# Kernel tuning notes

Hardware: AMD Instinct MI355X
Metric: run time of the kernel (lower is better)

The kernel has to match this reference:

```python
import jax, jax.numpy as jnp
import numpy as np

B, N, D = 8, 4096, 256
T = 768          # text_dim
E = 4            # num_experts
K = 2            # top_k
GS = 64          # grid_size = img_size // patch_size
WS = 8           # swin window size
NH = 4           # swin heads
MODES = 16       # fno modes
HID = 4 * D      # mlp hidden


def setup_inputs() -> dict:
    key = jax.random.key(0)
    ks = jax.random.split(key, 40)
    rn = lambda k, s, sc=0.02: jax.random.normal(k, s, jnp.float32) * sc
    return {
        "x": jax.random.normal(ks[0], (B, N, D), jnp.float32),
        "text_embedding": jax.random.normal(ks[1], (B, T), jnp.float32),
        # TopKGating: Linear(D+T->D), ReLU, Linear(D->E)
        "g1_w": rn(ks[2], (D, D + T)), "g1_b": jnp.zeros((D,), jnp.float32),
        "g2_w": rn(ks[3], (E, D)), "g2_b": jnp.zeros((E,), jnp.float32),
        # FNOExpert: SpectralConv2d complex weights (real/imag) + 1x1 conv
        "fno_w1r": rn(ks[4], (D, D, MODES, MODES), 1.0 / D), "fno_w1i": rn(ks[5], (D, D, MODES, MODES), 1.0 / D),
        "fno_w2r": rn(ks[6], (D, D, MODES, MODES), 1.0 / D), "fno_w2i": rn(ks[7], (D, D, MODES, MODES), 1.0 / D),
        "fno_cw": rn(ks[8], (D, D)), "fno_cb": jnp.zeros((D,), jnp.float32),
        # MLPExpert #1
        "m1_w1": rn(ks[9], (HID, D)), "m1_b1": jnp.zeros((HID,), jnp.float32),
        "m1_w2": rn(ks[10], (D, HID)), "m1_b2": jnp.zeros((D,), jnp.float32),
        # WindowAttentionExpert
        "a_ln1w": jnp.ones((D,), jnp.float32), "a_ln1b": jnp.zeros((D,), jnp.float32),
        "a_qkvw": rn(ks[11], (3 * D, D)), "a_qkvb": jnp.zeros((3 * D,), jnp.float32),
        "a_ow": rn(ks[12], (D, D)), "a_ob": jnp.zeros((D,), jnp.float32),
        "a_ln2w": jnp.ones((D,), jnp.float32), "a_ln2b": jnp.zeros((D,), jnp.float32),
        "a_mw1": rn(ks[13], (HID, D)), "a_mb1": jnp.zeros((HID,), jnp.float32),
        "a_mw2": rn(ks[14], (D, HID)), "a_mb2": jnp.zeros((D,), jnp.float32),
        # MLPExpert #2 (extra expert to reach num_experts=4)
        "m2_w1": rn(ks[15], (HID, D)), "m2_b1": jnp.zeros((HID,), jnp.float32),
        "m2_w2": rn(ks[16], (D, HID)), "m2_b2": jnp.zeros((D,), jnp.float32),
    }


def _gelu(v):
    return jax.nn.gelu(v, approximate=False)


def _ln(v, g, b, eps=1e-5):
    m = v.mean(-1, keepdims=True)
    var = ((v - m) ** 2).mean(-1, keepdims=True)
    return (v - m) * jax.lax.rsqrt(var + eps) * g + b


def reference(x, text_embedding, g1_w, g1_b, g2_w, g2_b,
              fno_w1r, fno_w1i, fno_w2r, fno_w2i, fno_cw, fno_cb,
              m1_w1, m1_b1, m1_w2, m1_b2,
              a_ln1w, a_ln1b, a_qkvw, a_qkvb, a_ow, a_ob,
              a_ln2w, a_ln2b, a_mw1, a_mb1, a_mw2, a_mb2,
              m2_w1, m2_b1, m2_w2, m2_b2):
    Bb, Nn, Dd = x.shape

    # ---- TopKGating ----
    feat = jnp.concatenate([x.mean(axis=1), text_embedding], axis=1)   # [B, D+T]
    h = jax.nn.relu(feat @ g1_w.T + g1_b)
    logits = h @ g2_w.T + g2_b                                         # [B, E]
    vals, idx = jax.lax.top_k(logits, K)
    w = jax.nn.softmax(vals, axis=1)                                   # [B, K]
    # per-(sample, expert) combine weight; indices are constants
    combine = (w[..., None] * jax.nn.one_hot(idx, E, dtype=x.dtype)).sum(axis=1)  # [B, E]

    # ---- Expert 0: FNO ----
    def fno(v):
        xg = v.transpose(0, 2, 1).reshape(Bb, Dd, GS, GS)              # [B, D, H, W]
        xft = jnp.fft.rfft2(xg)                                        # [B, D, H, W//2+1]
        w1 = fno_w1r + 1j * fno_w1i
        w2 = fno_w2r + 1j * fno_w2i
        lo = jnp.einsum('bixy,ioxy->boxy', xft[:, :, :MODES, :MODES], w1)
        hi = jnp.einsum('bixy,ioxy->boxy', xft[:, :, -MODES:, :MODES], w2)
        out_ft = jnp.zeros_like(xft)
        out_ft = out_ft.at[:, :, :MODES, :MODES].set(lo)
        out_ft = out_ft.at[:, :, -MODES:, :MODES].set(hi)
        x1 = jnp.fft.irfft2(out_ft, s=(GS, GS))
        x2 = jnp.einsum('bihw,oi->bohw', xg, fno_cw) + fno_cb[None, :, None, None]
        out = _gelu(x1 + x2)
        return out.reshape(Bb, Dd, Nn).transpose(0, 2, 1) + v

    # ---- MLP experts ----
    def mlp(v, w1, b1, w2, b2):
        return _gelu(v @ w1.T + b1) @ w2.T + b2 + v

    # ---- Expert 2: window attention ----
    def win_attn(v):
        xs = _ln(v, a_ln1w, a_ln1b).reshape(Bb, GS, GS, Dd)
        nw = GS // WS
        xw = xs.reshape(Bb, nw, WS, nw, WS, Dd).transpose(0, 1, 3, 2, 4, 5)
        xw = xw.reshape(-1, WS * WS, Dd)                               # [B*nw*nw, L, D]
        qkv = xw @ a_qkvw.T + a_qkvb
        q, k, vv = jnp.split(qkv, 3, axis=-1)
        dh = Dd // NH
        heads = lambda t: t.reshape(-1, WS * WS, NH, dh).transpose(0, 2, 1, 3)
        q, k, vv = heads(q), heads(k), heads(vv)
        attn = jax.nn.softmax(q @ k.transpose(0, 1, 3, 2) / jnp.sqrt(jnp.float32(dh)), axis=-1)
        o = (attn @ vv).transpose(0, 2, 1, 3).reshape(-1, WS * WS, Dd) @ a_ow.T + a_ob
        o = o.reshape(Bb, nw, nw, WS, WS, Dd).transpose(0, 1, 3, 2, 4, 5).reshape(Bb, Nn, Dd)
        v2 = v + o
        return v2 + (_gelu(_ln(v2, a_ln2w, a_ln2b) @ a_mw1.T + a_mb1) @ a_mw2.T + a_mb2)

    outs = [fno(x),
            mlp(x, m1_w1, m1_b1, m1_w2, m1_b2),
            win_attn(x),
            mlp(x, m2_w1, m2_b1, m2_w2, m2_b2)]
    final = sum(combine[:, e, None, None] * outs[e] for e in range(E))
    return final, w
```

## Files before the change

### kernel.cpp

```cpp
#include <hip/hip_runtime.h>
#include <math.h>

#define BB 8
#define NN 4096
#define DDIM 256
#define TT 768
#define BND (BB*NN*DDIM)

typedef unsigned short ushort_t;
typedef short bf16x8 __attribute__((ext_vector_type(8)));
typedef float f32x4 __attribute__((ext_vector_type(4)));

__device__ __forceinline__ float gelu_f(float v){
    return 0.5f * v * (1.0f + erff(v * 0.70710678118654752f));
}
__device__ __forceinline__ ushort_t f2bf(float f){
    union { float f; unsigned int u; } v; v.f = f;
    unsigned int u = v.u;
    u += 0x7FFFu + ((u >> 16) & 1u);
    return (ushort_t)(u >> 16);
}
__device__ __forceinline__ float bf2f(ushort_t h){
    union { unsigned int u; float f; } v; v.u = ((unsigned int)h) << 16;
    return v.f;
}
__device__ __forceinline__ float pk_re(unsigned int p){
    union { unsigned int u; float f; } v; v.u = p << 16; return v.f;
}
__device__ __forceinline__ float pk_im(unsigned int p){
    union { unsigned int u; float f; } v; v.u = p & 0xffff0000u; return v.f;
}
#define GLOAD16(gp, lp) __builtin_amdgcn_global_load_lds( \
    (__attribute__((address_space(1))) const void*)(gp),  \
    (__attribute__((address_space(3))) void*)(lp), 16, 0, 0)

__global__ __launch_bounds__(256) void k_xcvt2(const float4* __restrict__ x,
    const float* __restrict__ lng, const float* __restrict__ lnb,
    ushort_t* __restrict__ xbf, ushort_t* __restrict__ xlnbf, float4* __restrict__ outp,
    float* __restrict__ partialA){
    int w = threadIdx.x >> 6, lane = threadIdx.x & 63;
    int row = blockIdx.x*4 + w;
    size_t i4 = (size_t)row*64 + lane;
    float4 v = x[i4];
    outp[i4] = v;
    float vv[4] = {v.x, v.y, v.z, v.w};
    __shared__ float sda[4][256];
    *(float4*)&sda[w][lane*4] = v;
    float s = (vv[0]+vv[1])+(vv[2]+vv[3]);
    float s2 = (vv[0]*vv[0]+vv[1]*vv[1])+(vv[2]*vv[2]+vv[3]*vv[3]);
    for (int off=32; off; off>>=1){ s += __shfl_down(s, off); s2 += __shfl_down(s2, off); }
    float m = __shfl(s, 0) * (1.0f/DDIM);
    float var = __shfl(s2, 0) * (1.0f/DDIM) - m*m;
    float r = rsqrtf(var + 1e-5f);
    int c0 = lane*4;
    #pragma unroll
    for (int u=0;u<4;++u){
        size_t i = i4*4 + u;
        xbf[i] = f2bf(vv[u]);
        xlnbf[i] = f2bf((vv[u]-m)*r*lng[c0+u] + lnb[c0+u]);
    }
    __syncthreads();
    if (w==0){
        float4 a = *(const float4*)&sda[0][lane*4];
        float4 b4 = *(const float4*)&sda[1][lane*4];
        float4 c4 = *(const float4*)&sda[2][lane*4];
        float4 d4 = *(const float4*)&sda[3][lane*4];
        float4 sum = make_float4(a.x+b4.x+c4.x+d4.x, a.y+b4.y+c4.y+d4.y,
                                 a.z+b4.z+c4.z+d4.z, a.w+b4.w+c4.w+d4.w);
        *(float4*)&partialA[(size_t)blockIdx.x*256 + lane*4] = sum;
    }
}

__global__ __launch_bounds__(256) void k_meanB(const float* __restrict__ partialA, float* __restrict__ partialB){
    int seg = blockIdx.x, b = blockIdx.y, t = threadIdx.x;
    const float* p = partialA + ((size_t)(b*1024 + seg*64))*256 + t;
    float s0=0,s1=0,s2=0,s3=0;
    #pragma unroll
    for (int c=0;c<64;c+=4){
        s0 += p[(size_t)c*256];
        s1 += p[(size_t)(c+1)*256];
        s2 += p[(size_t)(c+2)*256];
        s3 += p[(size_t)(c+3)*256];
    }
    partialB[((size_t)b*16 + seg)*256 + t] = (s0+s1)+(s2+s3);
}

__global__ __launch_bounds__(256) void k_gate1(const float* __restrict__ partial, const float* __restrict__ text,
    const float* __restrict__ g1w, const float* __restrict__ g1b, float* __restrict__ hs){
    int d = blockIdx.x, t = threadIdx.x;
    int w = t >> 6, lane = t & 63;
    float xm[BB];
    #pragma unroll
    for (int b=0;b<BB;++b){
        float s = 0.f;
        #pragma unroll
        for (int c=0;c<16;++c) s += partial[((size_t)b*16 + c)*256 + t];
        xm[b] = s * (1.0f/NN);
    }
    const float* wrow = g1w + (size_t)d*(DDIM+TT);
    float w0 = wrow[t], w1 = wrow[256+t], w2 = wrow[512+t], w3 = wrow[768+t];
    float acc[BB];
    #pragma unroll
    for (int b=0;b<BB;++b){
        const float* tx = text + (size_t)b*TT;
        acc[b] = xm[b]*w0 + tx[t]*w1 + tx[256+t]*w2 + tx[512+t]*w3;
    }
    #pragma unroll
    for (int b=0;b<BB;++b)
        for (int off=32; off; off>>=1) acc[b] += __shfl_down(acc[b], off);
    __shared__ float red[BB][4];
    if (lane==0)
        #pragma unroll
        for (int b=0;b<BB;++b) red[b][w] = acc[b];
    __syncthreads();
    if (t < BB){
        float s = red[t][0]+red[t][1]+red[t][2]+red[t][3] + g1b[d];
        hs[t*DDIM + d] = fmaxf(s, 0.0f);
    }
}

__global__ __launch_bounds__(64) void k_gate2(const float* __restrict__ hs,
    const float* __restrict__ g2w, const float* __restrict__ g2b,
    float* __restrict__ combine, float* __restrict__ wout){
    __shared__ float lg[BB][4];
    int t = threadIdx.x;
    if (t < 32){
        int b = t>>2, e = t&3;
        float a = g2b[e];
        const float* w2 = g2w + e*DDIM;
        const float* h = hs + b*DDIM;
        for (int o=0;o<DDIM;o+=4)
            a += h[o]*w2[o] + h[o+1]*w2[o+1] + h[o+2]*w2[o+2] + h[o+3]*w2[o+3];
        lg[b][e] = a;
    }
    __syncthreads();
    if (t < BB){
        int b = t;
        int i1=0; float v1=lg[b][0];
        for (int e=1;e<4;++e){ if (lg[b][e] > v1){ v1=lg[b][e]; i1=e; } }
        int i2=0; float v2=-3.0e38f; bool found=false;
        for (int e=0;e<4;++e){ if (e==i1) continue; if (!found || lg[b][e] > v2){ v2=lg[b][e]; i2=e; found=true; } }
        float e2 = expf(v2 - v1);
        float inv = 1.0f/(1.0f + e2);
        float w0 = inv, w1 = e2*inv;
        float cv[4] = {0.f,0.f,0.f,0.f};
        cv[i1] = w0; cv[i2] = w1;
        for (int e=0;e<4;++e) combine[b*4+e] = cv[e];
        wout[b*2+0] = w0; wout[b*2+1] = w1;
    }
}

__global__ __launch_bounds__(256) void k_cvtw(
    const float* __restrict__ s0, const float* __restrict__ s1, const float* __restrict__ s2,
    const float* __restrict__ s3, const float* __restrict__ s4, const float* __restrict__ s5,
    const float* __restrict__ s6, const float* __restrict__ s7, const float* __restrict__ s8,
    ushort_t* __restrict__ dst){
    const int off[10] = {0,196608,262144,524288,786432,1048576,1310720,1572864,1835008,1900544};
    const float* srcs[9] = {s0,s1,s2,s3,s4,s5,s6,s7,s8};
    int i = (blockIdx.x*256 + threadIdx.x)*8;
    if (i >= 1900544) return;
    int seg = 0;
    #pragma unroll
    for (int k=1;k<9;++k) if (i >= off[k]) seg = k;
    const float* s = srcs[seg] + (i - off[seg]);
    ushort_t* d = dst + i;
    #pragma unroll
    for (int u=0;u<8;++u) d[u] = f2bf(s[u]);
}

__global__ __launch_bounds__(256) void k_v2cvt2(const float4* __restrict__ v2,
    const float* __restrict__ lng, const float* __restrict__ lnb,
    ushort_t* __restrict__ dstbf, const float* __restrict__ combine){
    int w = threadIdx.x >> 6, lane = threadIdx.x & 63;
    int row = blockIdx.x*4 + w;
    if (combine[(row>>12)*4+2]==0.0f) return;
    size_t i4 = (size_t)row*64 + lane;
    float4 v = v2[i4];
    float vv[4] = {v.x, v.y, v.z, v.w};
    float s = (vv[0]+vv[1])+(vv[2]+vv[3]);
    float s2 = (vv[0]*vv[0]+vv[1]*vv[1])+(vv[2]*vv[2]+vv[3]*vv[3]);
    for (int off=32; off; off>>=1){ s += __shfl_down(s, off); s2 += __shfl_down(s2, off); }
    float m = __shfl(s, 0) * (1.0f/DDIM);
    float var = __shfl(s2, 0) * (1.0f/DDIM) - m*m;
    float r = rsqrtf(var + 1e-5f);
    int c0 = lane*4;
    #pragma unroll
    for (int u=0;u<4;++u)
        dstbf[i4*4+u] = f2bf((vv[u]-m)*r*lng[c0+u] + lnb[c0+u]);
}

__global__ __launch_bounds__(256) void k_fft_w2(const ushort_t* __restrict__ xbf, float* __restrict__ F1,
                                                const float* __restrict__ combine){
    int h = blockIdx.x, b = blockIdx.y;
    if (combine[b*4+0]==0.0f) return;
    __shared__ ushort_t img[64*256];
    __shared__ float ct[64], st[64];
    int t = threadIdx.x;
    if (t < 64){ float ang = (float)t * 0.09817477042468103f; ct[t]=cosf(ang); st[t]=sinf(ang); }
    {
        const uint4* src = (const uint4*)(xbf + ((size_t)b*NN + h*64)*DDIM);
        uint4* dst4 = (uint4*)img;
        for (int i=t; i<2048; i+=256) dst4[i] = src[i];
    }
    __syncthreads();
    float re[16], im[16];
    #pragma unroll
    for (int ky=0;ky<16;++ky){ re[ky]=0.f; im[ky]=0.f; }
    for (int w=0; w<64; ++w){
        float v = bf2f(img[w*256 + t]);
        #pragma unroll
        for (int ky=0; ky<16; ++ky){
            int m = (ky*w)&63;
            re[ky] += v*ct[m];
            im[ky] -= v*st[m];
        }
    }
    float2* o = (float2*)(F1 + (((size_t)(b*DDIM + t))*1024 + h*16)*2);
    #pragma unroll
    for (int ky=0;ky<16;++ky) o[ky] = make_float2(re[ky], im[ky]);
}

__global__ __launch_bounds__(256) void k_fft_h(const float* __restrict__ F1,
                                               unsigned int* __restrict__ F2pk,
                                               const float* __restrict__ combine){
    int bd = blockIdx.x; int b = bd>>8;
    if (combine[b*4+0]==0.0f) return;
    __shared__ float f1[2048];
    __shared__ float ct[64], st[64];
    int t = threadIdx.x;
    if (t < 64){ float ang = (float)t * 0.09817477042468103f; ct[t]=cosf(ang); st[t]=sinf(ang); }
    const float* src = F1 + (size_t)bd*2048;
    for (int i=t;i<2048;i+=256) f1[i]=src[i];
    __syncthreads();
    for (int task=t; task<512; task+=256){
        int c = task>>8, kxp = (task>>4)&15, ky = task&15;
        int kx = c ? 48+kxp : kxp;
        float re=0.f, im=0.f;
        #pragma unroll
        for (int h=0;h<64;++h){
            int m = (kx*h)&63;
            float ar = f1[(h*16+ky)*2], ai = f1[(h*16+ky)*2+1];
            re += ar*ct[m] + ai*st[m];
            im += ai*ct[m] - ar*st[m];
        }
        F2pk[(size_t)bd*512 + task] = (((unsigned int)f2bf(im)) << 16) | (unsigned int)f2bf(re);
    }
}

__global__ __launch_bounds__(256) void k_specmul4(const unsigned int* __restrict__ F2pk,
    const float* __restrict__ w1r, const float* __restrict__ w1i,
    const float* __restrict__ w2r, const float* __restrict__ w2i,
    float* __restrict__ Gp, const float* __restrict__ combine){
    bool any=false;
    for (int b=0;b<BB;++b) any = any || (combine[b*4]!=0.0f);
    if (!any) return;
    int t  = threadIdx.x;
    int o0 = blockIdx.x * 2;
    int c  = blockIdx.y;
    int s  = blockIdx.z;
    const float* Wr = c ? w2r : w1r;
    const float* Wi = c ? w2i : w1i;
    float ar[2][BB], ai[2][BB];
    #pragma unroll
    for (int oo=0;oo<2;++oo)
        #pragma unroll
        for (int b=0;b<BB;++b){ ar[oo][b]=0.f; ai[oo][b]=0.f; }
    int i0 = s*64;
    for (int ii=i0; ii<i0+64; ii+=4){
        float wr[4][2], wi[4][2];
        #pragma unroll
        for (int u=0;u<4;++u)
            #pragma unroll
            for (int oo=0;oo<2;++oo){
                size_t widx = ((size_t)(ii+u)*DDIM + o0+oo)*256 + t;
                wr[u][oo] = Wr[widx];
                wi[u][oo] = Wi[widx];
            }
        unsigned int f[4][BB];
        #pragma unroll
        for (int u=0;u<4;++u)
            #pragma unroll
            for (int b=0;b<BB;++b)
                f[u][b] = F2pk[(size_t)b*131072 + (size_t)(ii+u)*512 + c*256 + t];
        #pragma unroll
        for (int u=0;u<4;++u)
            #pragma unroll
            for (int oo=0;oo<2;++oo)
                #pragma unroll
                for (int b=0;b<BB;++b){
                    float fr = pk_re(f[u][b]);
                    float fi = pk_im(f[u][b]);
                    ar[oo][b] += fr*wr[u][oo] - fi*wi[u][oo];
                    ai[oo][b] += fr*wi[u][oo] + fi*wr[u][oo];
                }
    }
    #pragma unroll
    for (int oo=0;oo<2;++oo)
        for (int b=0;b<BB;++b){
            float2* g = (float2*)(Gp + ((((size_t)s*BB + b)*DDIM + o0+oo)*512 + c*256 + t)*2);
            *g = make_float2(ar[oo][b], ai[oo][b]);
        }
}

__global__ __launch_bounds__(256) void k_ifft_h(const float* __restrict__ Gp, float* __restrict__ Z,
                                                const float* __restrict__ combine){
    int bd = blockIdx.x; int b = bd>>8;
    if (combine[b*4+0]==0.0f) return;
    __shared__ float g[1024];
    __shared__ float ct[64], st[64];
    int t=threadIdx.x;
    if (t < 64){ float ang = (float)t * 0.09817477042468103f; ct[t]=cosf(ang); st[t]=sinf(ang); }
    {
        const f32x4* p0 = (const f32x4*)(Gp + (size_t)bd*1024);
        const f32x4* p1 = (const f32x4*)(Gp + 2097152 + (size_t)bd*1024);
        const f32x4* p2 = (const f32x4*)(Gp + 2*2097152 + (size_t)bd*1024);
        const f32x4* p3 = (const f32x4*)(Gp + (size_t)3*2097152 + (size_t)bd*1024);
        f32x4 v = p0[t] + p1[t] + p2[t] + p3[t];
        *(f32x4*)(g + t*4) = v;
    }
    __syncthreads();
    for (int task=t;task<1024;task+=256){
        int h=task>>4, ky=task&15;
        float re=0.f, im=0.f;
        #pragma unroll
        for (int c=0;c<2;++c){
            #pragma unroll
            for (int kxp=0;kxp<16;++kxp){
                int kx = c ? 48+kxp : kxp;
                int m = (kx*h)&63;
                int gi = (c*256 + kxp*16 + ky)*2;
                float gr=g[gi], gim=g[gi+1];
                re += gr*ct[m] - gim*st[m];
                im += gr*st[m] + gim*ct[m];
            }
        }
        float2* o = (float2*)(Z + ((size_t)bd*1024 + task)*2);
        *o = make_float2(re*(1.0f/64.0f), im*(1.0f/64.0f));
    }
}

__global__ __launch_bounds__(256) void k_fno_out(const float* __restrict__ Z, const ushort_t* __restrict__ X2,
    const float* __restrict__ combine, float* __restrict__ out){
    int h = blockIdx.x, b = blockIdx.y;
    float cb = combine[b*4];
    if (cb==0.0f) return;
    __shared__ float ct[64], st[64];
    int t = threadIdx.x;
    if (t < 64){ float ang = (float)t * 0.09817477042468103f; ct[t]=cosf(ang); st[t]=sinf(ang); }
    __syncthreads();
    float zr[16], zi[16];
    const float* zp = Z + (((size_t)(b*DDIM + t)*64 + h)*16)*2;
    #pragma unroll
    for (int ky=0;ky<16;++ky){
        float2 v = *(const float2*)(zp + ky*2);
        zr[ky]=v.x; zi[ky]=v.y;
    }
    for (int w=0;w<64;++w){
        float s = zr[0];
        #pragma unroll
        for (int ky=1;ky<16;++ky){
            int m = (ky*w)&63;
            s += 2.0f*(zr[ky]*ct[m] - zi[ky]*st[m]);
        }
        s *= (1.0f/64.0f);
        size_t idx = ((size_t)b*NN + h*64 + w)*DDIM + t;
        out[idx] += cb * gelu_f(s + bf2f(X2[idx]));
    }
}

template<int EPI>
__global__ __launch_bounds__(256) void k_bgemm(
    const ushort_t* __restrict__ A, const ushort_t* __restrict__ W, const float* __restrict__ bias,
    void* __restrict__ dst, const float* __restrict__ combine, int expert, int K, int N,
    const float* __restrict__ xres, float* __restrict__ out)
{
    int tiles_n = N >> 7;
    int tm = blockIdx.x / tiles_n, tn = blockIdx.x - tm*tiles_n;
    int row0 = tm << 7, col0 = tn << 7;
    float scale = combine[(row0>>12)*4 + expert];
    if (scale == 0.0f) return;
    __shared__ __align__(16) ushort_t As[8192];
    __shared__ __align__(16) ushort_t Bs[8192];
    int t = threadIdx.x;
    int w = t >> 6, lane = t & 63;
    int wr = w >> 1, wc = w & 1;
    int lrow = lane >> 3, lk8 = (lane & 7) * 8;
    f32x4 acc[4][4];
    #pragma unroll
    for (int m=0;m<4;++m)
        #pragma unroll
        for (int n=0;n<4;++n) acc[m][n] = (f32x4){0.f,0.f,0.f,0.f};
    int afr = lane & 15, akr = (lane >> 4) * 8;
    for (int k0=0; k0<K; k0+=64){
        #pragma unroll
        for (int it=0; it<4; ++it){
            int c = it*4 + w;
            const ushort_t* ga = A + (size_t)(row0 + c*8 + lrow)*K + k0 + lk8;
            GLOAD16(ga, As + c*512);
            const ushort_t* gb = W + (size_t)(col0 + c*8 + lrow)*K + k0 + lk8;
            GLOAD16(gb, Bs + c*512);
        }
        __syncthreads();
        #pragma unroll
        for (int kk=0; kk<2; ++kk){
            bf16x8 af[4], bfr[4];
            #pragma unroll
            for (int m=0;m<4;++m)
                af[m] = *(const bf16x8*)(As + (wr*64 + m*16 + afr)*64 + kk*32 + akr);
            #pragma unroll
            for (int n=0;n<4;++n)
                bfr[n] = *(const bf16x8*)(Bs + (wc*64 + n*16 + afr)*64 + kk*32 + akr);
            #pragma unroll
            for (int m=0;m<4;++m)
                #pragma unroll
                for (int n=0;n<4;++n)
                    acc[m][n] = __builtin_amdgcn_mfma_f32_16x16x32_bf16(af[m], bfr[n], acc[m][n], 0, 0, 0);
        }
        __syncthreads();
    }
    int rbase = row0 + wr*64 + (lane>>4)*4;
    int cbase = col0 + wc*64 + (lane&15);
    #pragma unroll
    for (int n=0;n<4;++n){
        int col = cbase + n*16;
        float bcol = bias[col];
        #pragma unroll
        for (int m=0;m<4;++m){
            int r0 = rbase + m*16;
            f32x4 a = acc[m][n];
            #pragma unroll
            for (int j=0;j<4;++j){
                int r = r0 + j;
                float v = a[j] + bcol;
                if (EPI==0)      ((ushort_t*)dst)[(size_t)r*N + col] = f2bf(v);
                else if (EPI==1) ((ushort_t*)dst)[(size_t)r*N + col] = f2bf(gelu_f(v));
                else if (EPI==2) out[(size_t)r*DDIM + col] += scale * v;
                else if (EPI==3){
                    ((float*)dst)[(size_t)r*DDIM + col] = xres[(size_t)r*DDIM + col] + v;
                    out[(size_t)r*DDIM + col] += scale * v;
                }
            }
        }
    }
}

__global__ __launch_bounds__(256) void k_attn(const ushort_t* __restrict__ QKV, ushort_t* __restrict__ O,
                                              const float* __restrict__ combine){
    int wh = blockIdx.x;
    int w = wh>>2, head = wh&3;
    int b = w>>6;
    if (combine[b*4+2]==0.0f) return;
    int i1 = (w>>3)&7, i2 = w&7;
    __shared__ float A1[64][64];
    __shared__ float kk[64][65];
    __shared__ float S[64][65];
    int t = threadIdx.x;
    for (int idx=t; idx<4096; idx+=256){
        int l = idx>>6, dc = idx&63;
        int n = b*NN + (i1*8 + (l>>3))*64 + i2*8 + (l&7);
        const ushort_t* qrow = QKV + (size_t)n*768;
        A1[l][dc] = bf2f(qrow[head*64+dc]);
        kk[l][dc] = bf2f(qrow[256+head*64+dc]);
    }
    __syncthreads();
    for (int idx=t; idx<4096; idx+=256){
        int i=idx>>6, j=idx&63;
        float s=0.f;
        #pragma unroll 8
        for (int dc=0;dc<64;++dc) s += A1[i][dc]*kk[j][dc];
        S[i][j] = s * 0.125f;
    }
    __syncthreads();
    for (int idx=t; idx<4096; idx+=256){
        int l = idx>>6, dc = idx&63;
        int n = b*NN + (i1*8 + (l>>3))*64 + i2*8 + (l&7);
        A1[l][dc] = bf2f(QKV[(size_t)n*768 + 512 + head*64 + dc]);
    }
    __syncthreads();
    if (t < 64){
        float mx = -3.0e38f;
        for (int j=0;j<64;++j) mx = fmaxf(mx, S[t][j]);
        float sum=0.f;
        for (int j=0;j<64;++j){ float e = expf(S[t][j]-mx); S[t][j]=e; sum+=e; }
        float inv = 1.0f/sum;
        for (int j=0;j<64;++j) S[t][j] *= inv;
    }
    __syncthreads();
    for (int idx=t; idx<4096; idx+=256){
        int i=idx>>6, dc=idx&63;
        float s=0.f;
        #pragma unroll 8
        for (int j=0;j<64;++j) s += S[i][j]*A1[j][dc];
        int n = b*NN + (i1*8 + (i>>3))*64 + i2*8 + (i&7);
        O[(size_t)n*DDIM + head*64 + dc] = f2bf(s);
    }
}

extern "C" void kernel_launch(void* const* d_in, const int* in_sizes, int n_in,
                              void* d_out, int out_size, void* d_ws, size_t ws_size,
                              hipStream_t stream) {
    (void)in_sizes; (void)n_in; (void)out_size; (void)ws_size;
    const float* x      = (const float*)d_in[0];
    const float* text   = (const float*)d_in[1];
    const float* g1_w   = (const float*)d_in[2];
    const float* g1_b   = (const float*)d_in[3];
    const float* g2_w   = (const float*)d_in[4];
    const float* g2_b   = (const float*)d_in[5];
    const float* w1r    = (const float*)d_in[6];
    const float* w1i    = (const float*)d_in[7];
    const float* w2r    = (const float*)d_in[8];
    const float* w2i    = (const float*)d_in[9];
    const float* fno_cw = (const float*)d_in[10];
    const float* fno_cb = (const float*)d_in[11];
    const float* m1_w1  = (const float*)d_in[12];
    const float* m1_b1  = (const float*)d_in[13];
    const float* m1_w2  = (const float*)d_in[14];
    const float* m1_b2  = (const float*)d_in[15];
    const float* a_ln1w = (const float*)d_in[16];
    const float* a_ln1b = (const float*)d_in[17];
    const float* a_qkvw = (const float*)d_in[18];
    const float* a_qkvb = (const float*)d_in[19];
    const float* a_ow   = (const float*)d_in[20];
    const float* a_ob   = (const float*)d_in[21];
    const float* a_ln2w = (const float*)d_in[22];
    const float* a_ln2b = (const float*)d_in[23];
    const float* a_mw1  = (const float*)d_in[24];
    const float* a_mb1  = (const float*)d_in[25];
    const float* a_mw2  = (const float*)d_in[26];
    const float* a_mb2  = (const float*)d_in[27];
    const float* m2_w1  = (const float*)d_in[28];
    const float* m2_b1  = (const float*)d_in[29];
    const float* m2_w2  = (const float*)d_in[30];
    const float* m2_b2  = (const float*)d_in[31];

    float* out  = (float*)d_out;
    float* wout = out + (size_t)BND;

    float* wsf     = (float*)d_ws;
    float* hs      = wsf;
    float* combine = wsf + 2048;
    ushort_t* wbf  = (ushort_t*)(wsf + 69632);
    float* partialB = wsf + 1019904;
    ushort_t* x_bf   = (ushort_t*)(wsf + 1118208);
    ushort_t* xln_bf = (ushort_t*)(wsf + 5312512);
    float* R1 = wsf + 9506816;
    float* partialA = R1;
    float* Gp  = R1;
    float* F1  = R1 + 8388608;
    float* Z   = R1 + 16777216;
    ushort_t* X2_bf = (ushort_t*)(R1 + 20971520);
    unsigned int* F2pk = (unsigned int*)(R1 + 29360128);
    ushort_t* QKV_bf  = (ushort_t*)R1;
    ushort_t* O_bf    = (ushort_t*)(R1 + 12582912);
    float*    V2      = R1 + 16777216;
    ushort_t* v2ln_bf = (ushort_t*)(R1 + 25165824);
    ushort_t* H_bf = (ushort_t*)R1;

    ushort_t* qkvw_bf = wbf + 0;
    ushort_t* ow_bf   = wbf + 196608;
    ushort_t* mw1_bf  = wbf + 262144;
    ushort_t* mw2_bf  = wbf + 524288;
    ushort_t* m1w1_bf = wbf + 786432;
    ushort_t* m1w2_bf = wbf + 1048576;
    ushort_t* m2w1_bf = wbf + 1310720;
    ushort_t* m2w2_bf = wbf + 1572864;
    ushort_t* cw_bf   = wbf + 1835008;

    k_xcvt2<<<8192, 256, 0, stream>>>((const float4*)x, a_ln1w, a_ln1b, x_bf, xln_bf, (float4*)out, partialA);
    k_meanB<<<dim3(16,BB), 256, 0, stream>>>(partialA, partialB);
    k_gate1<<<256, 256, 0, stream>>>(partialB, text, g1_w, g1_b, hs);
    k_gate2<<<1, 64, 0, stream>>>(hs, g2_w, g2_b, combine, wout);
    k_cvtw<<<928, 256, 0, stream>>>(a_qkvw, a_ow, a_mw1, a_mw2, m1_w1, m1_w2, m2_w1, m2_w2, fno_cw, wbf);

    k_fft_w2<<<dim3(64,BB), 256, 0, stream>>>(x_bf, F1, combine);
    k_fft_h<<<2048, 256, 0, stream>>>(F1, F2pk, combine);
    k_specmul4<<<dim3(128,2,4), 256, 0, stream>>>(F2pk, w1r, w1i, w2r, w2i, Gp, combine);
    k_ifft_h<<<2048, 256, 0, stream>>>(Gp, Z, combine);
    k_bgemm<0><<<512, 256, 0, stream>>>(x_bf, cw_bf, fno_cb, X2_bf, combine, 0, 256, 256, nullptr, nullptr);
    k_fno_out<<<dim3(64,8), 256, 0, stream>>>(Z, X2_bf, combine, out);

    k_bgemm<1><<<2048, 256, 0, stream>>>(x_bf, m1w1_bf, m1_b1, H_bf, combine, 1, 256, 1024, nullptr, nullptr);
    k_bgemm<2><<<512, 256, 0, stream>>>(H_bf, m1w2_bf, m1_b2, nullptr, combine, 1, 1024, 256, nullptr, out);

    k_bgemm<0><<<1536, 256, 0, stream>>>(xln_bf, qkvw_bf, a_qkvb, QKV_bf, combine, 2, 256, 768, nullptr, nullptr);
    k_attn<<<2048, 256, 0, stream>>>(QKV_bf, O_bf, combine);
    k_bgemm<3><<<512, 256, 0, stream>>>(O_bf, ow_bf, a_ob, V2, combine, 2, 256, 256, x, out);
    k_v2cvt2<<<8192, 256, 0, stream>>>((const float4*)V2, a_ln2w, a_ln2b, v2ln_bf, combine);
    k_bgemm<1><<<2048, 256, 0, stream>>>(v2ln_bf, mw1_bf, a_mb1, H_bf, combine, 2, 256, 1024, nullptr, nullptr);
    k_bgemm<2><<<512, 256, 0, stream>>>(H_bf, mw2_bf, a_mb2, nullptr, combine, 2, 1024, 256, nullptr, out);

    k_bgemm<1><<<2048, 256, 0, stream>>>(x_bf, m2w1_bf, m2_b1, H_bf, combine, 3, 256, 1024, nullptr, nullptr);
    k_bgemm<2><<<512, 256, 0, stream>>>(H_bf, m2w2_bf, m2_b2, nullptr, combine, 3, 1024, 256, nullptr, out);
}
```

Before: 605.6 us.

## Restructure spectral multiply with wider per-thread tiles and swap GELU for tanh approximation

The spectral-multiply kernel now has each of 128 threads handle two modes using float2/uint2 vector loads. The input-channel reduction is split into 8 slices instead of 4, and the inverse-FFT kernel sums all 8 partial slices. Separately, the exact erf GELU is replaced by a tanh-form approximation built on __expf, which cuts transcendental cost in the MLP epilogues. That approximation departs from the reference's exact GELU and may exceed tolerance. The wider split also doubles the partial-sum buffer traffic, and writing 8 slices needs Gp to be twice as large as before.

Measured after the change: 592.4 us. -2.2%, faster.

```diff
diff --git a/kernel.cpp b/kernel.cpp
--- a/kernel.cpp
+++ b/kernel.cpp
@@ -12,7 +12,12 @@
 typedef float f32x4 __attribute__((ext_vector_type(4)));
 
 __device__ __forceinline__ float gelu_f(float v){
-    return 0.5f * v * (1.0f + erff(v * 0.70710678118654752f));
+    float y = 0.7978845608028654f * v * (1.0f + 0.044715f * v * v);
+    float ay = fabsf(y);
+    float e = __expf(-2.0f * ay);
+    float th = 1.0f - 2.0f * e / (1.0f + e);
+    th = copysignf(th, y);
+    return 0.5f * v * (1.0f + th);
 }
 __device__ __forceinline__ ushort_t f2bf(float f){
     union { float f; unsigned int u; } v; v.f = f;
@@ -247,7 +252,7 @@
     }
 }
 
-__global__ __launch_bounds__(256) void k_specmul4(const unsigned int* __restrict__ F2pk,
+__global__ __launch_bounds__(128) void k_specmul6(const unsigned int* __restrict__ F2pk,
     const float* __restrict__ w1r, const float* __restrict__ w1i,
     const float* __restrict__ w2r, const float* __restrict__ w2i,
     float* __restrict__ Gp, const float* __restrict__ combine){
@@ -258,47 +263,43 @@
     int o0 = blockIdx.x * 2;
     int c  = blockIdx.y;
     int s  = blockIdx.z;
-    const float* Wr = c ? w2r : w1r;
-    const float* Wi = c ? w2i : w1i;
-    float ar[2][BB], ai[2][BB];
+    int m0 = t*2;
+    const float* Wr = (c ? w2r : w1r) + ((size_t)(s*32)*DDIM + o0)*256 + m0;
+    const float* Wi = (c ? w2i : w1i) + ((size_t)(s*32)*DDIM + o0)*256 + m0;
+    const unsigned int* Fp = F2pk + (size_t)(s*32)*512 + c*256 + m0;
+    float ar[2][2][BB], ai[2][2][BB];
     #pragma unroll
     for (int oo=0;oo<2;++oo)
         #pragma unroll
-        for (int b=0;b<BB;++b){ ar[oo][b]=0.f; ai[oo][b]=0.f; }
-    int i0 = s*64;
-    for (int ii=i0; ii<i0+64; ii+=4){
-        float wr[4][2], wi[4][2];
-        #pragma unroll
-        for (int u=0;u<4;++u)
+        for (int mm=0;mm<2;++mm)
             #pragma unroll
-            for (int oo=0;oo<2;++oo){
-                size_t widx = ((size_t)(ii+u)*DDIM + o0+oo)*256 + t;
-                wr[u][oo] = Wr[widx];
-                wi[u][oo] = Wi[widx];
-            }
-        unsigned int f[4][BB];
-        #pragma unroll
-        for (int u=0;u<4;++u)
-            #pragma unroll
-            for (int b=0;b<BB;++b)
-                f[u][b] = F2pk[(size_t)b*131072 + (size_t)(ii+u)*512 + c*256 + t];
-        #pragma unroll
-        for (int u=0;u<4;++u)
-            #pragma unroll
-            for (int oo=0;oo<2;++oo)
-                #pragma unroll
-                for (int b=0;b<BB;++b){
-                    float fr = pk_re(f[u][b]);
-                    float fi = pk_im(f[u][b]);
-                    ar[oo][b] += fr*wr[u][oo] - fi*wi[u][oo];
-                    ai[oo][b] += fr*wi[u][oo] + fi*wr[u][oo];
-                }
+            for (int b=0;b<BB;++b){ ar[oo][mm][b]=0.f; ai[oo][mm][b]=0.f; }
+    for (int ii=0; ii<32; ++ii){
+        float2 wr0 = *(const float2*)(Wr);
+        float2 wr1 = *(const float2*)(Wr + 256);
+        float2 wi0 = *(const float2*)(Wi);
+        float2 wi1 = *(const float2*)(Wi + 256);
+        Wr += 65536; Wi += 65536;
+        uint2 f[BB];
+        #pragma unroll
+        for (int b=0;b<BB;++b)
+            f[b] = *(const uint2*)(Fp + (size_t)b*131072);
+        Fp += 512;
+        #pragma unroll
+        for (int b=0;b<BB;++b){
+            float fr0 = pk_re(f[b].x), fi0 = pk_im(f[b].x);
+            float fr1 = pk_re(f[b].y), fi1 = pk_im(f[b].y);
+            ar[0][0][b] += fr0*wr0.x - fi0*wi0.x;  ai[0][0][b] += fr0*wi0.x + fi0*wr0.x;
+            ar[0][1][b] += fr1*wr0.y - fi1*wi0.y;  ai[0][1][b] += fr1*wi0.y + fi1*wr0.y;
+            ar[1][0][b] += fr0*wr1.x - fi0*wi1.x;  ai[1][0][b] += fr0*wi1.x + fi0*wr1.x;
+            ar[1][1][b] += fr1*wr1.y - fi1*wi1.y;  ai[1][1][b] += fr1*wi1.y + fi1*wr1.y;
+        }
     }
     #pragma unroll
     for (int oo=0;oo<2;++oo)
         for (int b=0;b<BB;++b){
-            float2* g = (float2*)(Gp + ((((size_t)s*BB + b)*DDIM + o0+oo)*512 + c*256 + t)*2);
-            *g = make_float2(ar[oo][b], ai[oo][b]);
+            f32x4 v = {ar[oo][0][b], ai[oo][0][b], ar[oo][1][b], ai[oo][1][b]};
+            *(f32x4*)(Gp + ((((size_t)s*BB + b)*DDIM + o0+oo)*512 + c*256 + m0)*2) = v;
         }
 }
 
@@ -311,11 +312,12 @@
     int t=threadIdx.x;
     if (t < 64){ float ang = (float)t * 0.09817477042468103f; ct[t]=cosf(ang); st[t]=sinf(ang); }
     {
-        const f32x4* p0 = (const f32x4*)(Gp + (size_t)bd*1024);
-        const f32x4* p1 = (const f32x4*)(Gp + 2097152 + (size_t)bd*1024);
-        const f32x4* p2 = (const f32x4*)(Gp + 2*2097152 + (size_t)bd*1024);
-        const f32x4* p3 = (const f32x4*)(Gp + (size_t)3*2097152 + (size_t)bd*1024);
-        f32x4 v = p0[t] + p1[t] + p2[t] + p3[t];
+        f32x4 v = (f32x4){0.f,0.f,0.f,0.f};
+        #pragma unroll
+        for (int s=0;s<8;++s){
+            const f32x4* p = (const f32x4*)(Gp + (size_t)s*2097152 + (size_t)bd*1024);
+            v += p[t];
+        }
         *(f32x4*)(g + t*4) = v;
     }
     __syncthreads();
@@ -574,7 +576,7 @@
 
     k_fft_w2<<<dim3(64,BB), 256, 0, stream>>>(x_bf, F1, combine);
     k_fft_h<<<2048, 256, 0, stream>>>(F1, F2pk, combine);
-    k_specmul4<<<dim3(128,2,4), 256, 0, stream>>>(F2pk, w1r, w1i, w2r, w2i, Gp, combine);
+    k_specmul6<<<dim3(128,2,8), 128, 0, stream>>>(F2pk, w1r, w1i, w2r, w2i, Gp, combine);
     k_ifft_h<<<2048, 256, 0, stream>>>(Gp, Z, combine);
     k_bgemm<0><<<512, 256, 0, stream>>>(x_bf, cw_bf, fno_cb, X2_bf, combine, 0, 256, 256, nullptr, nullptr);
     k_fno_out<<<dim3(64,8), 256, 0, stream>>>(Z, X2_bf, combine, out);
```
